# Kernel tuning notes

Measured on AMD Instinct MI355X. Metric: run time of the kernel, lower is better.

Reference implementation:

```python
import jax, jax.numpy as jnp
import numpy as np

EPS = 1e-6

def _conv(x, w, padding):
    # x: [B,C,H,W], w: [O,I,kh,kw]
    return jax.lax.conv_general_dilated(x, w, window_strides=(1, 1), padding=padding,
                                        dimension_numbers=('NCHW', 'OIHW', 'NCHW'))

def setup_inputs() -> dict:
    key = jax.random.key(0)
    ks = jax.random.split(key, 8)
    C = 512
    B, H, W = 4, 64, 64
    s1 = 1.0 / np.sqrt(C)          # 1x1 conv fan-in
    s3 = 1.0 / np.sqrt(C * 9)      # 3x3 conv fan-in
    return {
        'x': jax.random.normal(ks[0], (B, C, H, W), dtype=jnp.float32),
        'ln_w': jnp.ones((C,), dtype=jnp.float32),
        'ln_b': jnp.zeros((C,), dtype=jnp.float32),
        'wq': jax.random.normal(ks[1], (C, C, 1, 1), dtype=jnp.float32) * s1,
        'wk': jax.random.normal(ks[2], (C, C, 3, 3), dtype=jnp.float32) * s3,
        'wv': jax.random.normal(ks[3], (C, C, 3, 3), dtype=jnp.float32) * s3,
        'wp': jax.random.normal(ks[4], (C, C, 1, 1), dtype=jnp.float32) * s1,
        'bp': jnp.zeros((C,), dtype=jnp.float32),
    }

def reference(x, ln_w, ln_b, wq, wk, wv, wp, bp):
    # channels_first LayerNorm over C
    u = jnp.mean(x, axis=1, keepdims=True)
    s = jnp.mean((x - u) ** 2, axis=1, keepdims=True)
    h = (x - u) / jnp.sqrt(s + EPS)
    h = ln_w[None, :, None, None] * h + ln_b[None, :, None, None]

    q = _conv(h, wq, 'VALID')           # 1x1
    k = _conv(h, wk, [(1, 1), (1, 1)])  # 3x3, pad 1
    v = _conv(h, wv, [(1, 1), (1, 1)])

    b, c, H, W = q.shape
    hw = H * W
    q = q.reshape(b, c, hw)
    k = k.reshape(b, c, hw)
    v = v.reshape(b, c, hw)

    scale = jnp.asarray(int(c) ** (-0.5), q.dtype)
    attn = jnp.einsum('bcm,bcn->bmn', q, k) * scale  # [b, hw_q, hw_k]
    attn = jax.nn.softmax(attn, axis=2)
    out = jnp.einsum('bcn,bmn->bcm', v, attn)        # [b, c, hw_q]
    out = out.reshape(b, c, H, W)

    out = _conv(out, wp, 'VALID') + bp[None, :, None, None]
    return x + out
```

## Files before the change

### kernel.cpp

```cpp
#include <hip/hip_runtime.h>
#include <hip/hip_bf16.h>

#define C_DIM 512
#define HW    4096
#define BATCH 4
#define PW    66
#define PPIX  (PW*PW)

typedef __attribute__((ext_vector_type(8))) short bf16x8;
typedef __attribute__((ext_vector_type(4))) float f32x4;
typedef __attribute__((ext_vector_type(16))) float f32x16;
typedef __attribute__((ext_vector_type(2))) long long l64x2;

static __device__ __forceinline__ short f2b(float f) {
    union { float f; unsigned u; } v; v.f = f;
    unsigned r = v.u + 0x7fffu + ((v.u >> 16) & 1u);
    return (short)(r >> 16);
}
static __device__ __forceinline__ float b2f(short s) {
    union { unsigned u; float f; } v; v.u = ((unsigned)(unsigned short)s) << 16;
    return v.f;
}

static __device__ __forceinline__ f32x4 zero4() {
    f32x4 v = {0.f, 0.f, 0.f, 0.f};
    return v;
}
static __device__ __forceinline__ f32x16 zero16() {
    f32x16 v = {0.f,0.f,0.f,0.f, 0.f,0.f,0.f,0.f, 0.f,0.f,0.f,0.f, 0.f,0.f,0.f,0.f};
    return v;
}

static __device__ __forceinline__ void gload16(const void* g, void* l) {
    __builtin_amdgcn_global_load_lds(
        (__attribute__((address_space(1))) void*)g,
        (__attribute__((address_space(3))) void*)l, 16, 0, 0);
}

__global__ void k_cvt_bf16(const float* __restrict__ in, short* __restrict__ out, int n) {
    int i = blockIdx.x * 256 + threadIdx.x;
    if (i < n) out[i] = f2b(in[i]);
}

__global__ void k_reorder_w3(const float* __restrict__ w, short* __restrict__ out) {
    int i = blockIdx.x * 256 + threadIdx.x;
    int c   = i & 511;
    int tap = (i >> 9) % 9;
    int o   = i / (9 * 512);
    out[i] = f2b(w[((size_t)o * 512 + c) * 9 + tap]);
}

__global__ void k_cvt_k8(const short* __restrict__ in, unsigned char* __restrict__ out) {
    int i = blockIdx.x * 256 + threadIdx.x;
    int m = i >> 6;
    int p = (i & 63) * 8;
    int kcp = p >> 6, g = (p >> 4) & 3, half = (p >> 3) & 1;
    int chb = (kcp * 2 + half) * 32 + g * 8;
    bf16x8 v = *(const bf16x8*)&in[(size_t)m * 512 + chb];
    int lo = __builtin_amdgcn_cvt_pk_fp8_f32(b2f(v[0]), b2f(v[1]), 0, false);
    lo     = __builtin_amdgcn_cvt_pk_fp8_f32(b2f(v[2]), b2f(v[3]), lo, true);
    int hi = __builtin_amdgcn_cvt_pk_fp8_f32(b2f(v[4]), b2f(v[5]), 0, false);
    hi     = __builtin_amdgcn_cvt_pk_fp8_f32(b2f(v[6]), b2f(v[7]), hi, true);
    *(uint2*)&out[(size_t)m * 512 + p] = make_uint2((unsigned)lo, (unsigned)hi);
}

__global__ void k_ln_fused(const float* __restrict__ x, const float* __restrict__ lnw,
                           const float* __restrict__ lnb, short* __restrict__ hp) {
    __shared__ float red[8][64];
    __shared__ float mean_s[64], rstd_s[64];
    __shared__ short tile[64][65];
    int bid = blockIdx.x;
    int y = bid & 63, b = bid >> 6;
    int t = threadIdx.x;
    int px = t & 63, cg = t >> 6;
    const float* xb = x + (size_t)b * C_DIM * HW + (size_t)y * 64;

    float s = 0.f, sq = 0.f;
    for (int c = cg * 128; c < cg * 128 + 128; ++c) {
        float v = xb[(size_t)c * HW + px];
        s += v; sq += v * v;
    }
    red[cg][px] = s;
    red[4 + cg][px] = sq;
    __syncthreads();
    if (t < 64) {
        float S = red[0][t] + red[1][t] + red[2][t] + red[3][t];
        float Q = red[4][t] + red[5][t] + red[6][t] + red[7][t];
        float mu  = S * (1.0f / C_DIM);
        float var = Q * (1.0f / C_DIM) - mu * mu;
        mean_s[t] = mu;
        rstd_s[t] = 1.0f / sqrtf(var + 1e-6f);
    }
    __syncthreads();
    float mu = mean_s[px], rs = rstd_s[px];
    int cj = t & 63, pj = t >> 6;
    for (int ct = 0; ct < 8; ++ct) {
        int c0 = ct * 64;
        #pragma unroll
        for (int cc = 0; cc < 64; cc += 4) {
            int c = c0 + cc + cg;
            float v = xb[(size_t)c * HW + px];
            tile[cc + cg][px] = f2b((v - mu) * rs * lnw[c] + lnb[c]);
        }
        __syncthreads();
        #pragma unroll
        for (int pp = 0; pp < 64; pp += 4) {
            int pidx = pp + pj;
            size_t dst = ((size_t)b * PPIX + (size_t)(y + 1) * PW + 1 + pidx) * C_DIM + c0 + cj;
            hp[dst] = tile[cj][pidx];
        }
        __syncthreads();
    }
}

template<int TAPS, int GMODE, int EPI>
__global__ __launch_bounds__(256, 2) void k_gemm(
        const short* __restrict__ A, const short* __restrict__ Bw,
        void* __restrict__ Out, const float* __restrict__ bias,
        const float* __restrict__ resid)
{
    constexpr int K = TAPS * 512;
    constexpr int NKC = K / 64;
    __shared__ short Alds[128 * 64];
    __shared__ short Blds[128 * 64];
    int bid = blockIdx.x;
    int mt = bid & 31, nt = (bid >> 5) & 3, b = bid >> 7;
    int m0 = mt * 128, n0 = nt * 128;
    int t = threadIdx.x;
    int lane = t & 63, w = t >> 6;
    int wm = w >> 1, wn = w & 1;
    int g = lane >> 4, li = lane & 15;
    int srow = t >> 3, schunk = t & 7;
    const short* Ab = A + (GMODE == 0 ? (size_t)b * PPIX * C_DIM : (size_t)b * HW * C_DIM);

    f32x4 acc[4][4];
    #pragma unroll
    for (int i = 0; i < 4; ++i)
        #pragma unroll
        for (int j = 0; j < 4; ++j) acc[i][j] = zero4();

    for (int kc = 0; kc < NKC; ++kc) {
        int tap = (TAPS == 9) ? (kc >> 3) : 4;
        int cb  = (kc & 7) * 64;
        __syncthreads();
        #pragma unroll
        for (int r = 0; r < 4; ++r) {
            int row = r * 32 + srow;
            size_t goff;
            if (GMODE == 0) {
                int m = m0 + row;
                int yy = m >> 6, xx = m & 63;
                int pp = (yy + tap / 3) * PW + xx + (tap % 3);
                goff = (size_t)pp * C_DIM + cb + schunk * 8;
            } else {
                goff = (size_t)(m0 + row) * K + kc * 64 + schunk * 8;
            }
            gload16(Ab + goff, Alds + row * 64 + schunk * 8);
        }
        #pragma unroll
        for (int r = 0; r < 4; ++r) {
            int row = r * 32 + srow;
            size_t goff = (size_t)(n0 + row) * K + kc * 64 + schunk * 8;
            gload16(Bw + goff, Blds + row * 64 + schunk * 8);
        }
        __syncthreads();
        #pragma unroll
        for (int ks = 0; ks < 2; ++ks) {
            int koff = ks * 32 + g * 8;
            bf16x8 af[4], bfr[4];
            #pragma unroll
            for (int i = 0; i < 4; ++i)
                af[i] = *(const bf16x8*)&Alds[(wm * 64 + i * 16 + li) * 64 + koff];
            #pragma unroll
            for (int j = 0; j < 4; ++j)
                bfr[j] = *(const bf16x8*)&Blds[(wn * 64 + j * 16 + li) * 64 + koff];
            #pragma unroll
            for (int i = 0; i < 4; ++i)
                #pragma unroll
                for (int j = 0; j < 4; ++j)
                    acc[i][j] = __builtin_amdgcn_mfma_f32_16x16x32_bf16(af[i], bfr[j], acc[i][j], 0, 0, 0);
        }
    }
    #pragma unroll
    for (int fm = 0; fm < 4; ++fm) {
        #pragma unroll
        for (int fn = 0; fn < 4; ++fn) {
            int mrow = m0 + wm * 64 + fm * 16 + g * 4;
            int ncol = n0 + wn * 64 + fn * 16 + li;
            if constexpr (EPI == 0) {
                #pragma unroll
                for (int i = 0; i < 4; ++i) {
                    size_t dst = ((size_t)b * HW + mrow + i) * C_DIM + ncol;
                    ((short*)Out)[dst] = f2b(acc[fm][fn][i]);
                }
            } else if constexpr (EPI == 1) {
                size_t dst = ((size_t)b * C_DIM + ncol) * HW + mrow;
                short4 sv = make_short4(f2b(acc[fm][fn][0]), f2b(acc[fm][fn][1]),
                                        f2b(acc[fm][fn][2]), f2b(acc[fm][fn][3]));
                *(short4*)((short*)Out + dst) = sv;
            } else {
                size_t dst = ((size_t)b * C_DIM + ncol) * HW + mrow;
                float bb = bias[ncol];
                float4 xr = *(const float4*)(resid + dst);
                float4 o;
                o.x = acc[fm][fn][0] + bb + xr.x;
                o.y = acc[fm][fn][1] + bb + xr.y;
                o.z = acc[fm][fn][2] + bb + xr.z;
                o.w = acc[fm][fn][3] + bb + xr.w;
                *(float4*)((float*)Out + dst) = o;
            }
        }
    }
}

__global__ __launch_bounds__(256, 2) void k_gemm_kv2(
        const short* __restrict__ A, const short* __restrict__ Bk,
        const short* __restrict__ Bv, short* __restrict__ OutK,
        short* __restrict__ OutV)
{
    constexpr int K = 4608;
    __shared__ short Alds[2][5120];
    __shared__ short Bklds[2][5120];
    __shared__ short Bvlds[2][5120];
    int bid = blockIdx.x;
    int mt = bid & 31, nt = (bid >> 5) & 3, b = bid >> 7;
    int m0 = mt * 128, n0 = nt * 128;
    int t = threadIdx.x;
    int lane = t & 63, w = t >> 6;
    int wm = w >> 1, wn = w & 1;
    int g = lane >> 4, li = lane & 15;
    const short* Ab = A + (size_t)b * PPIX * C_DIM;

    int srowv[3], schv[3];
    #pragma unroll
    for (int r = 0; r < 3; ++r) {
        int slot = r * 256 + t;
        int row = slot / 5;
        int ch = slot - row * 5;
        srowv[r] = row;
        schv[r] = (ch < 4) ? ch * 8 : 0;
    }
    bool act2 = (w < 2);

    f32x4 accK[4][4], accV[4][4];
    #pragma unroll
    for (int i = 0; i < 4; ++i)
        #pragma unroll
        for (int j = 0; j < 4; ++j) { accK[i][j] = zero4(); accV[i][j] = zero4(); }

    auto STAGE = [&](int bf, int kc2) {
        int tap = kc2 >> 4;
        int cofs = (kc2 & 15) * 32;
        int ty3 = tap / 3, tx3 = tap % 3;
        #pragma unroll
        for (int r = 0; r < 3; ++r) {
            if (r < 2 || act2) {
                int row = srowv[r];
                int m = m0 + row;
                int yy = m >> 6, xx = m & 63;
                int pp = (yy + ty3) * PW + xx + tx3;
                int dst = (r * 256 + t) * 8;
                gload16(Ab + (size_t)pp * C_DIM + cofs + schv[r], &Alds[bf][dst]);
                size_t gb = (size_t)(n0 + row) * K + tap * 512 + cofs + schv[r];
                gload16(Bk + gb, &Bklds[bf][dst]);
                gload16(Bv + gb, &Bvlds[bf][dst]);
            }
        }
    };

    auto COMPUTE = [&](int bf) {
        bf16x8 af[4], bk[4], bv[4];
        #pragma unroll
        for (int i = 0; i < 4; ++i)
            af[i] = *(const bf16x8*)&Alds[bf][(wm * 64 + i * 16 + li) * 40 + g * 8];
        #pragma unroll
        for (int j = 0; j < 4; ++j)
            bk[j] = *(const bf16x8*)&Bklds[bf][(wn * 64 + j * 16 + li) * 40 + g * 8];
        #pragma unroll
        for (int i = 0; i < 4; ++i)
            #pragma unroll
            for (int j = 0; j < 4; ++j)
                accK[i][j] = __builtin_amdgcn_mfma_f32_16x16x32_bf16(af[i], bk[j], accK[i][j], 0, 0, 0);
        #pragma unroll
        for (int j = 0; j < 4; ++j)
            bv[j] = *(const bf16x8*)&Bvlds[bf][(wn * 64 + j * 16 + li) * 40 + g * 8];
        #pragma unroll
        for (int i = 0; i < 4; ++i)
            #pragma unroll
            for (int j = 0; j < 4; ++j)
                accV[i][j] = __builtin_amdgcn_mfma_f32_16x16x32_bf16(af[i], bv[j], accV[i][j], 0, 0, 0);
    };

    STAGE(0, 0);
    __syncthreads();
    int bf = 0;
    for (int kc2 = 0; kc2 < 144; ++kc2) {
        if (kc2 + 1 < 144) STAGE(bf ^ 1, kc2 + 1);
        COMPUTE(bf);
        __syncthreads();
        bf ^= 1;
    }

    #pragma unroll
    for (int fm = 0; fm < 4; ++fm) {
        #pragma unroll
        for (int fn = 0; fn < 4; ++fn) {
            int mrow = m0 + wm * 64 + fm * 16 + g * 4;
            int ncol = n0 + wn * 64 + fn * 16 + li;
            #pragma unroll
            for (int i = 0; i < 4; ++i) {
                size_t dst = ((size_t)b * HW + mrow + i) * C_DIM + ncol;
                OutK[dst] = f2b(accK[fm][fn][i]);
            }
            size_t dstv = ((size_t)b * C_DIM + ncol) * HW + mrow;
            short4 sv = make_short4(f2b(accV[fm][fn][0]), f2b(accV[fm][fn][1]),
                                    f2b(accV[fm][fn][2]), f2b(accV[fm][fn][3]));
            *(short4*)(OutV + dstv) = sv;
        }
    }
}

#define KT 32
#define NTILES 64
__global__ __launch_bounds__(512, 2) void k_attn(
        const short* __restrict__ qT, const unsigned char* __restrict__ kT8,
        const short* __restrict__ vg, short* __restrict__ O0,
        short* __restrict__ O1, float* __restrict__ L0, float* __restrict__ L1)
{
    __shared__ __align__(16) short pool[73728];
    unsigned char* Kp8 = (unsigned char*)pool;
    short* Vp = pool + 16384;
    short* Pp = pool + 57344;

    int bid0 = blockIdx.x;
    int bid = (bid0 & 7) * 32 + (bid0 >> 3);
    int qt = bid & 31, ks = (bid >> 5) & 1, b = bid >> 6;
    int m0 = qt * 128;
    int t = threadIdx.x, lane = t & 63, w = t >> 6;
    int g = lane >> 4, li = lane & 15;
    int l31 = lane & 31, l5 = lane >> 5;

    const unsigned char* kb8 = kT8 + ((size_t)b * HW + (size_t)ks * 2048) * 512;
    const short* vb = vg + (size_t)b * C_DIM * HW + ks * 2048;

    long long qf8[16];
    {
        const short* qrow = qT + ((size_t)b * HW + m0 + w * 16 + li) * C_DIM;
        #pragma unroll
        for (int kc = 0; kc < 16; ++kc) {
            bf16x8 qv = *(const bf16x8*)&qrow[kc * 32 + g * 8];
            int lo = __builtin_amdgcn_cvt_pk_fp8_f32(b2f(qv[0]), b2f(qv[1]), 0, false);
            lo     = __builtin_amdgcn_cvt_pk_fp8_f32(b2f(qv[2]), b2f(qv[3]), lo, true);
            int hi = __builtin_amdgcn_cvt_pk_fp8_f32(b2f(qv[4]), b2f(qv[5]), 0, false);
            hi     = __builtin_amdgcn_cvt_pk_fp8_f32(b2f(qv[6]), b2f(qv[7]), hi, true);
            qf8[kc] = ((long long)(unsigned)hi << 32) | (unsigned)lo;
        }
    }
    f32x16 oacc[8];
    #pragma unroll
    for (int a = 0; a < 8; ++a) oacc[a] = zero16();
    float lsum = 0.f;

    const unsigned char* ksrc8 = kb8 + (size_t)(t & 31) * 512 + (t >> 5) * 16;
    int voff[5];
    #pragma unroll
    for (int r = 0; r < 5; ++r) {
        int D = r * 512 + t;
        int ch = D / 5;
        int c  = D - ch * 5;
        voff[r] = (c < 4) ? ch * 4096 + c * 8 : 0;
    }

    const float SC = 0.044194173824159216f * 1.4426950408889634f;

    auto STAGE = [&](int buf, int nt) {
        int n0 = nt * KT;
        const unsigned char* kS = ksrc8 + (size_t)n0 * 512;
        unsigned char* kD = Kp8 + buf * 16384 + t * 16;
        gload16(kS, kD);
        gload16(kS + 256, kD + 8192);
        short* vD = Vp + buf * 20480 + t * 8;
        #pragma unroll
        for (int r = 0; r < 5; ++r)
            gload16(vb + voff[r] + n0, vD + r * 4096);
    };

    STAGE(0, 0);
    asm volatile("s_waitcnt vmcnt(0)" ::: "memory");
    __builtin_amdgcn_s_barrier();
    __builtin_amdgcn_sched_barrier(0);

    int buf = 0;
    for (int nt = 0; nt < NTILES; ++nt) {
        if (nt + 1 < NTILES) STAGE(buf ^ 1, nt + 1);

        const unsigned char* kbase8 = Kp8 + buf * 16384 + g * 512 + li * 16;
        f32x4 s0[2], s1[2];
        s0[0] = zero4(); s0[1] = zero4(); s1[0] = zero4(); s1[1] = zero4();
        __builtin_amdgcn_s_setprio(1);
        #pragma unroll
        for (int kcp = 0; kcp < 8; ++kcp) {
            #pragma unroll
            for (int fn = 0; fn < 2; ++fn) {
                l64x2 kv = *(const l64x2*)&kbase8[kcp * 2048 + fn * 256];
                s0[fn] = __builtin_amdgcn_mfma_f32_16x16x32_fp8_fp8(kv[0], qf8[2 * kcp],     s0[fn], 0, 0, 0);
                s1[fn] = __builtin_amdgcn_mfma_f32_16x16x32_fp8_fp8(kv[1], qf8[2 * kcp + 1], s1[fn], 0, 0, 0);
            }
        }
        __builtin_amdgcn_s_setprio(0);
        #pragma unroll
        for (int fn = 0; fn < 2; ++fn) {
            float e0 = exp2f((s0[fn][0] + s1[fn][0]) * SC);
            float e1 = exp2f((s0[fn][1] + s1[fn][1]) * SC);
            float e2 = exp2f((s0[fn][2] + s1[fn][2]) * SC);
            float e3 = exp2f((s0[fn][3] + s1[fn][3]) * SC);
            lsum += (e0 + e1) + (e2 + e3);
            union { __hip_bfloat162 h; unsigned u; } p01, p23;
            p01.h = __float22bfloat162_rn(make_float2(e0, e1));
            p23.h = __float22bfloat162_rn(make_float2(e2, e3));
            *(uint2*)&Pp[(w * 16 + li) * 40 + fn * 16 + g * 4] = make_uint2(p01.u, p23.u);
        }

        asm volatile("s_waitcnt lgkmcnt(0)" ::: "memory");
        __builtin_amdgcn_s_barrier();
        __builtin_amdgcn_sched_barrier(0);

        const short* vbase = Vp + buf * 20480 + (size_t)w * 64 * 40;
        bf16x8 vf[2][2];
        #pragma unroll
        for (int cht = 0; cht < 2; ++cht)
            #pragma unroll
            for (int kx = 0; kx < 2; ++kx)
                vf[cht][kx] = *(const bf16x8*)&vbase[(cht * 32 + l31) * 40 + kx * 16 + l5 * 8];
        __builtin_amdgcn_s_setprio(1);
        #pragma unroll
        for (int q2 = 0; q2 < 4; ++q2) {
            #pragma unroll
            for (int kx = 0; kx < 2; ++kx) {
                bf16x8 pf = *(const bf16x8*)&Pp[(q2 * 32 + l31) * 40 + kx * 16 + l5 * 8];
                oacc[q2 * 2 + 0] = __builtin_amdgcn_mfma_f32_32x32x16_bf16(vf[0][kx], pf, oacc[q2 * 2 + 0], 0, 0, 0);
                oacc[q2 * 2 + 1] = __builtin_amdgcn_mfma_f32_32x32x16_bf16(vf[1][kx], pf, oacc[q2 * 2 + 1], 0, 0, 0);
            }
        }
        __builtin_amdgcn_s_setprio(0);

        asm volatile("s_waitcnt vmcnt(0)" ::: "memory");
        __builtin_amdgcn_s_barrier();
        __builtin_amdgcn_sched_barrier(0);
        buf ^= 1;
    }

    lsum += __shfl_xor(lsum, 16);
    lsum += __shfl_xor(lsum, 32);
    float* Lb = (ks ? L1 : L0) + (size_t)b * HW + m0 + w * 16;
    if (lane < 16) Lb[lane] = lsum;

    short* tp = pool + w * 9216;
    #pragma unroll
    for (int a = 0; a < 8; ++a) {
        int q2 = a >> 1, cht = a & 1;
        int q_l = q2 * 32 + l31;
        #pragma unroll
        for (int rq = 0; rq < 4; ++rq) {
            int chb = cht * 32 + rq * 8 + l5 * 4;
            union { __hip_bfloat162 h; unsigned u; } x01, x23;
            x01.h = __float22bfloat162_rn(make_float2(oacc[a][rq * 4 + 0], oacc[a][rq * 4 + 1]));
            x23.h = __float22bfloat162_rn(make_float2(oacc[a][rq * 4 + 2], oacc[a][rq * 4 + 3]));
            *(uint2*)&tp[q_l * 72 + chb] = make_uint2(x01.u, x23.u);
        }
    }
    asm volatile("s_waitcnt lgkmcnt(0)" ::: "memory");
    __builtin_amdgcn_sched_barrier(0);
    short* Ob = (ks ? O1 : O0) + ((size_t)b * HW + m0) * C_DIM + w * 64;
    #pragma unroll
    for (int qg = 0; qg < 16; ++qg) {
        int qr = qg * 8 + (lane >> 3);
        bf16x8 v = *(const bf16x8*)&tp[qr * 72 + (lane & 7) * 8];
        *(bf16x8*)&Ob[(size_t)qr * C_DIM + (lane & 7) * 8] = v;
    }
}

__global__ void k_att_comb(const short* __restrict__ O0, const short* __restrict__ O1,
                           const float* __restrict__ L0, const float* __restrict__ L1,
                           short* __restrict__ oatt) {
    int i = blockIdx.x * 256 + threadIdx.x;
    int row = i >> 6;
    int c0 = (i & 63) * 8;
    float r = 1.0f / (L0[row] + L1[row]);
    size_t base = (size_t)row * C_DIM + c0;
    bf16x8 a = *(const bf16x8*)&O0[base];
    bf16x8 c = *(const bf16x8*)&O1[base];
    bf16x8 o;
    #pragma unroll
    for (int j = 0; j < 8; ++j)
        o[j] = f2b((b2f(a[j]) + b2f(c[j])) * r);
    *(bf16x8*)&oatt[base] = o;
}

extern "C" void kernel_launch(void* const* d_in, const int* in_sizes, int n_in,
                              void* d_out, int out_size, void* d_ws, size_t ws_size,
                              hipStream_t stream) {
    const float* x    = (const float*)d_in[0];
    const float* ln_w = (const float*)d_in[1];
    const float* ln_b = (const float*)d_in[2];
    const float* wq   = (const float*)d_in[3];
    const float* wk   = (const float*)d_in[4];
    const float* wv   = (const float*)d_in[5];
    const float* wp   = (const float*)d_in[6];
    const float* bp   = (const float*)d_in[7];
    float* out = (float*)d_out;

    char* ws = (char*)d_ws;
    size_t off = 0;
    auto alloc = [&](size_t bytes) {
        char* p = ws + off;
        off += (bytes + 255) & ~(size_t)255;
        return p;
    };
    short* hp   = (short*)alloc((size_t)BATCH * PPIX * C_DIM * 2);
    short* wqb  = (short*)alloc((size_t)512 * 512 * 2);
    short* wkr  = (short*)alloc((size_t)512 * 4608 * 2);
    short* wvr  = (short*)alloc((size_t)512 * 4608 * 2);
    short* wpb  = (short*)alloc((size_t)512 * 512 * 2);
    short* qT   = (short*)alloc((size_t)BATCH * HW * C_DIM * 2);
    short* kT   = (short*)alloc((size_t)BATCH * HW * C_DIM * 2);
    short* vg   = (short*)alloc((size_t)BATCH * HW * C_DIM * 2);
    short* oatt = (short*)alloc((size_t)BATCH * HW * C_DIM * 2);
    float* mean = (float*)alloc((size_t)BATCH * HW * 4);
    float* rstd = (float*)alloc((size_t)BATCH * HW * 4);

    hipMemsetAsync(hp, 0, (size_t)BATCH * PPIX * C_DIM * 2, stream);
    k_cvt_bf16<<<1024, 256, 0, stream>>>(wq, wqb, 512 * 512);
    k_cvt_bf16<<<1024, 256, 0, stream>>>(wp, wpb, 512 * 512);
    k_reorder_w3<<<9216, 256, 0, stream>>>(wk, wkr);
    k_reorder_w3<<<9216, 256, 0, stream>>>(wv, wvr);
    k_ln_fused<<<256, 256, 0, stream>>>(x, ln_w, ln_b, hp);

    k_gemm<1, 0, 0><<<512, 256, 0, stream>>>(hp, wqb, qT, nullptr, nullptr);
    k_gemm_kv2<<<512, 256, 0, stream>>>(hp, wkr, wvr, kT, vg);

    unsigned char* kT8 = (unsigned char*)wkr;
    k_cvt_k8<<<4096, 256, 0, stream>>>(kT, kT8);

    short* Op0 = hp;
    short* Op1 = oatt;
    float* Ls0 = mean;
    float* Ls1 = rstd;
    k_attn<<<256, 512, 0, stream>>>(qT, kT8, vg, Op0, Op1, Ls0, Ls1);
    k_att_comb<<<4096, 256, 0, stream>>>(Op0, Op1, Ls0, Ls1, oatt);

    k_gemm<1, 1, 2><<<512, 256, 0, stream>>>(oatt, wpb, out, bp, x);
}
```

Measured before the change: 393.8 us.

## Run 3x3 K/V convolution GEMM in FP8 with scaled weights

The fused K/V 3x3 convolution GEMM now takes FP8 operands: weights are scaled by 64 and packed to FP8 in the MFMA k-layout, and the padded LayerNorm output is converted to FP8 by a new kernel. The GEMM uses fp8 MFMA with half as many K iterations and rescales the accumulators on output. This cuts operand bandwidth and doubles MFMA throughput on the largest GEMM, at the cost of an extra conversion pass over the activations and lower precision in K and V.

```diff
diff --git a/kernel.cpp b/kernel.cpp
--- a/kernel.cpp
+++ b/kernel.cpp
@@ -42,12 +42,39 @@
     if (i < n) out[i] = f2b(in[i]);
 }
 
-__global__ void k_reorder_w3(const float* __restrict__ w, short* __restrict__ out) {
+__global__ void k_reorder_w38(const float* __restrict__ w, unsigned char* __restrict__ out) {
     int i = blockIdx.x * 256 + threadIdx.x;
-    int c   = i & 511;
-    int tap = (i >> 9) % 9;
-    int o   = i / (9 * 512);
-    out[i] = f2b(w[((size_t)o * 512 + c) * 9 + tap]);
+    int o = i / 576;
+    int p8 = (i - o * 576) * 8;
+    int kc2 = p8 >> 6;
+    int tap = kc2 >> 3;
+    int p = p8 & 63;
+    int g = (p >> 4) & 3, half = (p >> 3) & 1;
+    int c0 = (kc2 & 7) * 64 + half * 32 + g * 8;
+    const float* src = w + ((size_t)o * 512 + c0) * 9 + tap;
+    float f0 = src[0] * 64.f, f1 = src[9] * 64.f, f2 = src[18] * 64.f, f3 = src[27] * 64.f;
+    float f4 = src[36] * 64.f, f5 = src[45] * 64.f, f6 = src[54] * 64.f, f7 = src[63] * 64.f;
+    int lo = __builtin_amdgcn_cvt_pk_fp8_f32(f0, f1, 0, false);
+    lo     = __builtin_amdgcn_cvt_pk_fp8_f32(f2, f3, lo, true);
+    int hi = __builtin_amdgcn_cvt_pk_fp8_f32(f4, f5, 0, false);
+    hi     = __builtin_amdgcn_cvt_pk_fp8_f32(f6, f7, hi, true);
+    *(uint2*)&out[(size_t)o * 4608 + p8] = make_uint2((unsigned)lo, (unsigned)hi);
+}
+
+__global__ void k_cvt_h8(const short* __restrict__ hp, unsigned char* __restrict__ out) {
+    int i = blockIdx.x * 256 + threadIdx.x;
+    int row = i >> 6;
+    int p8 = (i & 63) * 8;
+    int grp = p8 >> 6;
+    int p = p8 & 63;
+    int g = (p >> 4) & 3, half = (p >> 3) & 1;
+    int c = grp * 64 + half * 32 + g * 8;
+    bf16x8 v = *(const bf16x8*)&hp[(size_t)row * 512 + c];
+    int lo = __builtin_amdgcn_cvt_pk_fp8_f32(b2f(v[0]), b2f(v[1]), 0, false);
+    lo     = __builtin_amdgcn_cvt_pk_fp8_f32(b2f(v[2]), b2f(v[3]), lo, true);
+    int hi = __builtin_amdgcn_cvt_pk_fp8_f32(b2f(v[4]), b2f(v[5]), 0, false);
+    hi     = __builtin_amdgcn_cvt_pk_fp8_f32(b2f(v[6]), b2f(v[7]), hi, true);
+    *(uint2*)&out[(size_t)row * 512 + p8] = make_uint2((unsigned)lo, (unsigned)hi);
 }
 
 __global__ void k_cvt_k8(const short* __restrict__ in, unsigned char* __restrict__ out) {
@@ -213,15 +240,14 @@
     }
 }
 
-__global__ __launch_bounds__(256, 2) void k_gemm_kv2(
-        const short* __restrict__ A, const short* __restrict__ Bk,
-        const short* __restrict__ Bv, short* __restrict__ OutK,
+__global__ __launch_bounds__(256, 2) void k_gemm_kv8(
+        const unsigned char* __restrict__ A8, const unsigned char* __restrict__ Bk8,
+        const unsigned char* __restrict__ Bv8, short* __restrict__ OutK,
         short* __restrict__ OutV)
 {
-    constexpr int K = 4608;
-    __shared__ short Alds[2][5120];
-    __shared__ short Bklds[2][5120];
-    __shared__ short Bvlds[2][5120];
+    __shared__ unsigned char Alds[2][10240];
+    __shared__ unsigned char Bklds[2][10240];
+    __shared__ unsigned char Bvlds[2][10240];
     int bid = blockIdx.x;
     int mt = bid & 31, nt = (bid >> 5) & 3, b = bid >> 7;
     int m0 = mt * 128, n0 = nt * 128;
@@ -229,7 +255,7 @@
     int lane = t & 63, w = t >> 6;
     int wm = w >> 1, wn = w & 1;
     int g = lane >> 4, li = lane & 15;
-    const short* Ab = A + (size_t)b * PPIX * C_DIM;
+    const unsigned char* Ab = A8 + (size_t)b * PPIX * 512;
 
     int srowv[3], schv[3];
     #pragma unroll
@@ -238,7 +264,7 @@
         int row = slot / 5;
         int ch = slot - row * 5;
         srowv[r] = row;
-        schv[r] = (ch < 4) ? ch * 8 : 0;
+        schv[r] = (ch < 4) ? ch * 16 : 0;
     }
     bool act2 = (w < 2);
 
@@ -249,8 +275,8 @@
         for (int j = 0; j < 4; ++j) { accK[i][j] = zero4(); accV[i][j] = zero4(); }
 
     auto STAGE = [&](int bf, int kc2) {
-        int tap = kc2 >> 4;
-        int cofs = (kc2 & 15) * 32;
+        int tap = kc2 >> 3;
+        int gofs = (kc2 & 7) * 64;
         int ty3 = tap / 3, tx3 = tap % 3;
         #pragma unroll
         for (int r = 0; r < 3; ++r) {
@@ -259,48 +285,54 @@
                 int m = m0 + row;
                 int yy = m >> 6, xx = m & 63;
                 int pp = (yy + ty3) * PW + xx + tx3;
-                int dst = (r * 256 + t) * 8;
-                gload16(Ab + (size_t)pp * C_DIM + cofs + schv[r], &Alds[bf][dst]);
-                size_t gb = (size_t)(n0 + row) * K + tap * 512 + cofs + schv[r];
-                gload16(Bk + gb, &Bklds[bf][dst]);
-                gload16(Bv + gb, &Bvlds[bf][dst]);
+                int dst = (r * 256 + t) * 16;
+                gload16(Ab + (size_t)pp * 512 + gofs + schv[r], &Alds[bf][dst]);
+                size_t gb = (size_t)(n0 + row) * 4608 + kc2 * 64 + schv[r];
+                gload16(Bk8 + gb, &Bklds[bf][dst]);
+                gload16(Bv8 + gb, &Bvlds[bf][dst]);
             }
         }
     };
 
     auto COMPUTE = [&](int bf) {
-        bf16x8 af[4], bk[4], bv[4];
+        l64x2 av[4], bk[4], bv[4];
         #pragma unroll
         for (int i = 0; i < 4; ++i)
-            af[i] = *(const bf16x8*)&Alds[bf][(wm * 64 + i * 16 + li) * 40 + g * 8];
+            av[i] = *(const l64x2*)&Alds[bf][(wm * 64 + i * 16 + li) * 80 + g * 16];
         #pragma unroll
         for (int j = 0; j < 4; ++j)
-            bk[j] = *(const bf16x8*)&Bklds[bf][(wn * 64 + j * 16 + li) * 40 + g * 8];
-        #pragma unroll
-        for (int i = 0; i < 4; ++i)
-            #pragma unroll
-            for (int j = 0; j < 4; ++j)
-                accK[i][j] = __builtin_amdgcn_mfma_f32_16x16x32_bf16(af[i], bk[j], accK[i][j], 0, 0, 0);
+            bk[j] = *(const l64x2*)&Bklds[bf][(wn * 64 + j * 16 + li) * 80 + g * 16];
         #pragma unroll
         for (int j = 0; j < 4; ++j)
-            bv[j] = *(const bf16x8*)&Bvlds[bf][(wn * 64 + j * 16 + li) * 40 + g * 8];
-        #pragma unroll
-        for (int i = 0; i < 4; ++i)
-            #pragma unroll
-            for (int j = 0; j < 4; ++j)
-                accV[i][j] = __builtin_amdgcn_mfma_f32_16x16x32_bf16(af[i], bv[j], accV[i][j], 0, 0, 0);
+            bv[j] = *(const l64x2*)&Bvlds[bf][(wn * 64 + j * 16 + li) * 80 + g * 16];
+        #pragma unroll
+        for (int h = 0; h < 2; ++h) {
+            #pragma unroll
+            for (int i = 0; i < 4; ++i)
+                #pragma unroll
+                for (int j = 0; j < 4; ++j)
+                    accK[i][j] = __builtin_amdgcn_mfma_f32_16x16x32_fp8_fp8(
+                        av[i][h], bk[j][h], accK[i][j], 0, 0, 0);
+            #pragma unroll
+            for (int i = 0; i < 4; ++i)
+                #pragma unroll
+                for (int j = 0; j < 4; ++j)
+                    accV[i][j] = __builtin_amdgcn_mfma_f32_16x16x32_fp8_fp8(
+                        av[i][h], bv[j][h], accV[i][j], 0, 0, 0);
+        }
     };
 
     STAGE(0, 0);
     __syncthreads();
     int bf = 0;
-    for (int kc2 = 0; kc2 < 144; ++kc2) {
-        if (kc2 + 1 < 144) STAGE(bf ^ 1, kc2 + 1);
+    for (int kc2 = 0; kc2 < 72; ++kc2) {
+        if (kc2 + 1 < 72) STAGE(bf ^ 1, kc2 + 1);
         COMPUTE(bf);
         __syncthreads();
         bf ^= 1;
     }
 
+    const float SCL = 0.015625f;
     #pragma unroll
     for (int fm = 0; fm < 4; ++fm) {
         #pragma unroll
@@ -310,11 +342,11 @@
             #pragma unroll
             for (int i = 0; i < 4; ++i) {
                 size_t dst = ((size_t)b * HW + mrow + i) * C_DIM + ncol;
-                OutK[dst] = f2b(accK[fm][fn][i]);
+                OutK[dst] = f2b(accK[fm][fn][i] * SCL);
             }
             size_t dstv = ((size_t)b * C_DIM + ncol) * HW + mrow;
-            short4 sv = make_short4(f2b(accV[fm][fn][0]), f2b(accV[fm][fn][1]),
-                                    f2b(accV[fm][fn][2]), f2b(accV[fm][fn][3]));
+            short4 sv = make_short4(f2b(accV[fm][fn][0] * SCL), f2b(accV[fm][fn][1] * SCL),
+                                    f2b(accV[fm][fn][2] * SCL), f2b(accV[fm][fn][3] * SCL));
             *(short4*)(OutV + dstv) = sv;
         }
     }
@@ -518,9 +550,10 @@
         return p;
     };
     short* hp   = (short*)alloc((size_t)BATCH * PPIX * C_DIM * 2);
+    unsigned char* hp8 = (unsigned char*)alloc((size_t)BATCH * PPIX * 512);
     short* wqb  = (short*)alloc((size_t)512 * 512 * 2);
-    short* wkr  = (short*)alloc((size_t)512 * 4608 * 2);
-    short* wvr  = (short*)alloc((size_t)512 * 4608 * 2);
+    unsigned char* wk8 = (unsigned char*)alloc((size_t)512 * 4608);
+    unsigned char* wv8 = (unsigned char*)alloc((size_t)512 * 4608);
     short* wpb  = (short*)alloc((size_t)512 * 512 * 2);
     short* qT   = (short*)alloc((size_t)BATCH * HW * C_DIM * 2);
     short* kT   = (short*)alloc((size_t)BATCH * HW * C_DIM * 2);
@@ -532,14 +565,15 @@
     hipMemsetAsync(hp, 0, (size_t)BATCH * PPIX * C_DIM * 2, stream);
     k_cvt_bf16<<<1024, 256, 0, stream>>>(wq, wqb, 512 * 512);
     k_cvt_bf16<<<1024, 256, 0, stream>>>(wp, wpb, 512 * 512);
-    k_reorder_w3<<<9216, 256, 0, stream>>>(wk, wkr);
-    k_reorder_w3<<<9216, 256, 0, stream>>>(wv, wvr);
+    k_reorder_w38<<<1152, 256, 0, stream>>>(wk, wk8);
+    k_reorder_w38<<<1152, 256, 0, stream>>>(wv, wv8);
     k_ln_fused<<<256, 256, 0, stream>>>(x, ln_w, ln_b, hp);
+    k_cvt_h8<<<4356, 256, 0, stream>>>(hp, hp8);
 
     k_gemm<1, 0, 0><<<512, 256, 0, stream>>>(hp, wqb, qT, nullptr, nullptr);
-    k_gemm_kv2<<<512, 256, 0, stream>>>(hp, wkr, wvr, kT, vg);
-
-    unsigned char* kT8 = (unsigned char*)wkr;
+    k_gemm_kv8<<<512, 256, 0, stream>>>(hp8, wk8, wv8, kT, vg);
+
+    unsigned char* kT8 = hp8;
     k_cvt_k8<<<4096, 256, 0, stream>>>(kT, kT8);
 
     short* Op0 = hp;
```

Result: faster. 340.4 us (-13.6%).
